# Kernel optimization log

Hardware: AMD Instinct MI355X
Metric: run time of the kernel (lower is better)

## Reference

```python
import jax, jax.numpy as jnp
import numpy as np

MARGIN = 0.2
NEG_INF = -1e30


def setup_inputs() -> dict:
    key = jax.random.key(0)
    k1, k2 = jax.random.split(key)
    B, D, C = 384, 256, 48
    features = jax.random.normal(k1, (B, D), dtype=jnp.float32)
    labels = jax.random.randint(k2, (B,), 0, C, dtype=jnp.int32)
    return {"features": features, "labels": labels, "epoch": 5}


def reference(features, labels, epoch):
    B = features.shape[0]
    # pairwise euclidean distance, clamped like torch.clamp(min=1e-11)
    diff = features[:, None, :] - features[None, :, :]          # [B,B,D]
    dist = jnp.sqrt(jnp.clip(jnp.sum(diff * diff, axis=-1), 1e-11))  # [B,B]

    idx = jnp.arange(B)
    same = labels[:, None] == labels[None, :]
    pos_mask = same & (idx[None, :] > idx[:, None])             # pairs (i,j), j>i, same label
    neg_mask = ~same

    # Gumbel-max sampling replaces the per-row np.random.choice host loop.
    gumbel = jax.random.gumbel(jax.random.key(42), (B, B, B), dtype=dist.dtype)

    if epoch > 3:
        # semi-hard negatives: pos_dist < d(i,k) < pos_dist + margin, weights 1/d(i,k)
        d_ik = dist[:, None, :]                                 # [B,1,B]
        d_pos = dist[:, :, None]                                # [B,B,1]
        semi = neg_mask[:, None, :] & (d_ik > d_pos) & (d_ik < d_pos + MARGIN)  # [B,B,B]
        logits = jnp.where(semi, -jnp.log(dist)[:, None, :], NEG_INF)  # log(1/d)
        has_neg = jnp.any(semi, axis=-1)                        # [B,B]
    else:
        # uniform random negative per (i,j) pair
        logits = jnp.where(neg_mask[:, None, :], 0.0, NEG_INF)  # [B,1,B]
        has_neg = jnp.broadcast_to(jnp.any(neg_mask, axis=-1)[:, None], (B, B))

    neg_idx = jnp.argmax(logits + gumbel, axis=-1)              # [B,B]
    neg_dist = jnp.take_along_axis(dist, neg_idx, axis=1)       # d(i, sampled_neg)

    valid = pos_mask & has_neg
    # MarginRankingLoss(neg, pos, target=1) = relu(pos - neg + margin)
    per_pair = jax.nn.relu(dist - neg_dist + MARGIN)
    count = jnp.sum(valid)
    total = jnp.sum(jnp.where(valid, per_pair, 0.0))
    return jnp.where(count > 0, total / jnp.maximum(count, 1), 0.0)
```

## Files before the change

kernel.cpp:

```cpp
#include <hip/hip_runtime.h>
#include <hip/hip_bf16.h>
#include <stdint.h>

#define BSZ 384
#define DD  256
#define NWAVES 6
#define NEG_BIG -3.0e38f

__device__ __forceinline__ void threefry_0_42(uint32_t c0, uint32_t c1,
                                              uint32_t& o0, uint32_t& o1) {
    const uint32_t k0 = 0u;
    const uint32_t k1 = 42u;
    const uint32_t k2 = 0u ^ 42u ^ 0x1BD11BDAu;
    uint32_t x0 = c0 + k0;
    uint32_t x1 = c1 + k1;
#define TF_RND(R) { x0 += x1; x1 = (x1 << (R)) | (x1 >> (32 - (R))); x1 ^= x0; }
    TF_RND(13) TF_RND(15) TF_RND(26) TF_RND(6)
    x0 += k1; x1 += k2 + 1u;
    TF_RND(17) TF_RND(29) TF_RND(16) TF_RND(24)
    x0 += k2; x1 += k0 + 2u;
    TF_RND(13) TF_RND(15) TF_RND(26) TF_RND(6)
    x0 += k0; x1 += k1 + 3u;
    TF_RND(17) TF_RND(29) TF_RND(16) TF_RND(24)
    x0 += k1; x1 += k2 + 4u;
    TF_RND(13) TF_RND(15) TF_RND(26) TF_RND(6)
    x0 += k2; x1 += k0 + 5u;
#undef TF_RND
    o0 = x0; o1 = x1;
}

__device__ __forceinline__ float gumbel_at(uint32_t idx) {
    uint32_t r0, r1;
    threefry_0_42(0u, idx, r0, r1);
    uint32_t bits = r0 ^ r1;
    uint32_t mant = bits >> 9;
    float f = __uint_as_float(mant | 0x3F800000u) - 1.0f;
    float u = (mant == 0u) ? 1.17549435e-38f : f;
    return -logf(-logf(u));
}

__global__ __launch_bounds__(BSZ) void fused_kernel(const float* __restrict__ F,
                                                    const int* __restrict__ labels,
                                                    const int* __restrict__ epochp,
                                                    float* __restrict__ total,
                                                    unsigned int* __restrict__ count,
                                                    unsigned int* __restrict__ done,
                                                    float* __restrict__ out) {
    __shared__ float    row[BSZ];
    __shared__ float    nlog[BSZ];
    __shared__ int      slab[BSZ];
    __shared__ int      plist[BSZ];
    __shared__ int      npos;
    __shared__ float    wtot[NWAVES];
    __shared__ unsigned wcnt[NWAVES];

    const int i    = blockIdx.x;
    const int tid  = threadIdx.x;
    const int wave = tid >> 6;
    const int lane = tid & 63;
    const int rl   = lane >> 3;
    const int s    = lane & 7;

    slab[tid] = labels[tid];
    if (tid == 0) npos = 0;
    __syncthreads();

    const int lab_i = slab[i];
    if (tid > i && slab[tid] == lab_i)
        plist[atomicAdd(&npos, 1)] = tid;
    const int  epoch   = *epochp;
    const bool semisel = (epoch > 3);
    __syncthreads();

    const int np = npos;
    float    t_total = 0.0f;
    unsigned t_count = 0u;

    if (np > 0) {
        const float4* F4 = (const float4*)F;

        float4 fi[8];
#pragma unroll
        for (int t = 0; t < 8; ++t) fi[t] = F4[i * (DD / 4) + t * 8 + s];

        for (int c = 0; c < 8; ++c) {
            const int k = c * 48 + wave * 8 + rl;
            const float4* fk = F4 + (size_t)k * (DD / 4);
            float a0 = 0.f, a1 = 0.f, a2 = 0.f, a3 = 0.f;
#pragma unroll
            for (int t = 0; t < 8; ++t) {
                float4 b = fk[t * 8 + s];
                float d0 = fi[t].x - b.x;
                float d1 = fi[t].y - b.y;
                float d2 = fi[t].z - b.z;
                float d3 = fi[t].w - b.w;
                a0 = fmaf(d0, d0, a0);
                a1 = fmaf(d1, d1, a1);
                a2 = fmaf(d2, d2, a2);
                a3 = fmaf(d3, d3, a3);
            }
            float p = (a0 + a1) + (a2 + a3);
            p += __shfl_down(p, 4, 64);
            p += __shfl_down(p, 2, 64);
            p += __shfl_down(p, 1, 64);
            if (s == 0) row[k] = sqrtf(fmaxf(p, 1e-11f));
        }
        __syncthreads();
        nlog[tid] = semisel ? -logf(row[tid]) : 0.0f;
        __syncthreads();

        for (int p = wave; p < np; p += NWAVES) {
            const int   j     = plist[p];
            const float d_pos = row[j];
            const float hi    = d_pos + 0.2f;
            float v  = NEG_BIG;
            int   kk = 0;
#pragma unroll
            for (int c = 0; c < BSZ / 64; ++c) {
                const int   k   = c * 64 + lane;
                const float dkk = row[k];
                const bool cand = (slab[k] != lab_i) &&
                                  (!semisel || (dkk > d_pos && dkk < hi));
                if (__any(cand)) {
                    if (cand) {
                        const uint32_t idx = (uint32_t)(i * BSZ + j) * (uint32_t)BSZ
                                             + (uint32_t)k;
                        float val = nlog[k] + gumbel_at(idx);
                        if (val > v) { v = val; kk = k; }
                    }
                }
            }
#pragma unroll
            for (int off = 32; off; off >>= 1) {
                float ov = __shfl_down(v, off, 64);
                int   oi = __shfl_down(kk, off, 64);
                if (ov > v || (ov == v && oi < kk)) { v = ov; kk = oi; }
            }
            if (lane == 0 && v > -1.0e38f) {
                t_total += fmaxf(d_pos - row[kk] + 0.2f, 0.0f);
                t_count += 1u;
            }
        }
    }

    if (lane == 0) { wtot[wave] = t_total; wcnt[wave] = t_count; }
    __syncthreads();
    if (tid == 0) {
        float    tt = 0.0f;
        unsigned cc = 0u;
#pragma unroll
        for (int q = 0; q < NWAVES; ++q) { tt += wtot[q]; cc += wcnt[q]; }
        if (cc) {
            atomicAdd(total, tt);
            atomicAdd(count, cc);
        }
        __threadfence();
        const unsigned prev = atomicAdd(done, 1u);
        if (prev == (unsigned)gridDim.x - 1u) {
            const float    T = atomicAdd(total, 0.0f);
            const unsigned C = atomicAdd(count, 0u);
            out[0] = (C > 0u) ? (T / (float)C) : 0.0f;
        }
    }
}

extern "C" void kernel_launch(void* const* d_in, const int* in_sizes, int n_in,
                              void* d_out, int out_size, void* d_ws, size_t ws_size,
                              hipStream_t stream) {
    const float* F      = (const float*)d_in[0];
    const int*   labels = (const int*)d_in[1];
    const int*   epoch  = (const int*)d_in[2];
    float*       out    = (float*)d_out;

    if (ws_size < 12) return;
    float*        total = (float*)d_ws;
    unsigned int* count = (unsigned int*)d_ws + 1;
    unsigned int* done  = (unsigned int*)d_ws + 2;

    hipMemsetAsync(d_ws, 0, 12, stream);
    fused_kernel<<<BSZ, BSZ, 0, stream>>>(F, labels, epoch, total, count, done, out);
}
```

Measured before the change: 79.01 us.

## Process two anchors per block and replace atomics with a reduction kernel

Each block now handles two anchor rows, so every loaded feature row k is reused for two distance computations. This halves the grid to 192 blocks and combines the positive-pair work of both anchors into one list. The global atomic accumulation, done-counter and memset are replaced by per-block slots plus a second single-wave reduction kernel. The costs are an extra kernel launch, higher register use, and fewer blocks to spread the Gumbel sampling work across the GPU.

```diff
diff --git a/kernel.cpp b/kernel.cpp
--- a/kernel.cpp
+++ b/kernel.cpp
@@ -5,6 +5,8 @@
 #define BSZ 384
 #define DD  256
 #define NWAVES 6
+#define NANCH 2
+#define NBLK (BSZ / NANCH)
 #define NEG_BIG -3.0e38f
 
 __device__ __forceinline__ void threefry_0_42(uint32_t c0, uint32_t c1,
@@ -42,19 +44,17 @@
 __global__ __launch_bounds__(BSZ) void fused_kernel(const float* __restrict__ F,
                                                     const int* __restrict__ labels,
                                                     const int* __restrict__ epochp,
-                                                    float* __restrict__ total,
-                                                    unsigned int* __restrict__ count,
-                                                    unsigned int* __restrict__ done,
-                                                    float* __restrict__ out) {
-    __shared__ float    row[BSZ];
-    __shared__ float    nlog[BSZ];
+                                                    float* __restrict__ tot_slot,
+                                                    unsigned int* __restrict__ cnt_slot) {
+    __shared__ float    row[NANCH][BSZ];
+    __shared__ float    nlog[NANCH][BSZ];
     __shared__ int      slab[BSZ];
-    __shared__ int      plist[BSZ];
+    __shared__ int      plist[NANCH * BSZ];
     __shared__ int      npos;
     __shared__ float    wtot[NWAVES];
     __shared__ unsigned wcnt[NWAVES];
 
-    const int i    = blockIdx.x;
+    const int i0   = blockIdx.x * NANCH;
     const int tid  = threadIdx.x;
     const int wave = tid >> 6;
     const int lane = tid & 63;
@@ -65,9 +65,10 @@
     if (tid == 0) npos = 0;
     __syncthreads();
 
-    const int lab_i = slab[i];
-    if (tid > i && slab[tid] == lab_i)
-        plist[atomicAdd(&npos, 1)] = tid;
+    const int lab0 = slab[i0];
+    const int lab1 = slab[i0 + 1];
+    if (tid > i0     && slab[tid] == lab0) plist[atomicAdd(&npos, 1)] = tid;
+    if (tid > i0 + 1 && slab[tid] == lab1) plist[atomicAdd(&npos, 1)] = (1 << 16) | tid;
     const int  epoch   = *epochp;
     const bool semisel = (epoch > 3);
     __syncthreads();
@@ -79,53 +80,65 @@
     if (np > 0) {
         const float4* F4 = (const float4*)F;
 
-        float4 fi[8];
-#pragma unroll
-        for (int t = 0; t < 8; ++t) fi[t] = F4[i * (DD / 4) + t * 8 + s];
+        float4 f0[8], f1[8];
+#pragma unroll
+        for (int t = 0; t < 8; ++t) {
+            f0[t] = F4[(i0    ) * (DD / 4) + t * 8 + s];
+            f1[t] = F4[(i0 + 1) * (DD / 4) + t * 8 + s];
+        }
 
         for (int c = 0; c < 8; ++c) {
             const int k = c * 48 + wave * 8 + rl;
             const float4* fk = F4 + (size_t)k * (DD / 4);
-            float a0 = 0.f, a1 = 0.f, a2 = 0.f, a3 = 0.f;
+            float a00 = 0.f, a01 = 0.f, a02 = 0.f, a03 = 0.f;
+            float a10 = 0.f, a11 = 0.f, a12 = 0.f, a13 = 0.f;
 #pragma unroll
             for (int t = 0; t < 8; ++t) {
                 float4 b = fk[t * 8 + s];
-                float d0 = fi[t].x - b.x;
-                float d1 = fi[t].y - b.y;
-                float d2 = fi[t].z - b.z;
-                float d3 = fi[t].w - b.w;
-                a0 = fmaf(d0, d0, a0);
-                a1 = fmaf(d1, d1, a1);
-                a2 = fmaf(d2, d2, a2);
-                a3 = fmaf(d3, d3, a3);
-            }
-            float p = (a0 + a1) + (a2 + a3);
-            p += __shfl_down(p, 4, 64);
-            p += __shfl_down(p, 2, 64);
-            p += __shfl_down(p, 1, 64);
-            if (s == 0) row[k] = sqrtf(fmaxf(p, 1e-11f));
+                float d0 = f0[t].x - b.x, d1 = f0[t].y - b.y;
+                float d2 = f0[t].z - b.z, d3 = f0[t].w - b.w;
+                a00 = fmaf(d0, d0, a00); a01 = fmaf(d1, d1, a01);
+                a02 = fmaf(d2, d2, a02); a03 = fmaf(d3, d3, a03);
+                float e0 = f1[t].x - b.x, e1 = f1[t].y - b.y;
+                float e2 = f1[t].z - b.z, e3 = f1[t].w - b.w;
+                a10 = fmaf(e0, e0, a10); a11 = fmaf(e1, e1, a11);
+                a12 = fmaf(e2, e2, a12); a13 = fmaf(e3, e3, a13);
+            }
+            float p0 = (a00 + a01) + (a02 + a03);
+            float p1 = (a10 + a11) + (a12 + a13);
+            p0 += __shfl_down(p0, 4, 64); p1 += __shfl_down(p1, 4, 64);
+            p0 += __shfl_down(p0, 2, 64); p1 += __shfl_down(p1, 2, 64);
+            p0 += __shfl_down(p0, 1, 64); p1 += __shfl_down(p1, 1, 64);
+            if (s == 0) {
+                row[0][k] = sqrtf(fmaxf(p0, 1e-11f));
+                row[1][k] = sqrtf(fmaxf(p1, 1e-11f));
+            }
         }
         __syncthreads();
-        nlog[tid] = semisel ? -logf(row[tid]) : 0.0f;
+        nlog[0][tid] = semisel ? -logf(row[0][tid]) : 0.0f;
+        nlog[1][tid] = semisel ? -logf(row[1][tid]) : 0.0f;
         __syncthreads();
 
         for (int p = wave; p < np; p += NWAVES) {
-            const int   j     = plist[p];
-            const float d_pos = row[j];
+            const int   pl    = plist[p];
+            const int   a     = pl >> 16;
+            const int   j     = pl & 0xFFFF;
+            const int   lab_a = a ? lab1 : lab0;
+            const float* rwa  = row[a];
+            const float d_pos = rwa[j];
             const float hi    = d_pos + 0.2f;
+            const uint32_t jb = (uint32_t)((i0 + a) * BSZ + j) * (uint32_t)BSZ;
             float v  = NEG_BIG;
             int   kk = 0;
 #pragma unroll
             for (int c = 0; c < BSZ / 64; ++c) {
                 const int   k   = c * 64 + lane;
-                const float dkk = row[k];
-                const bool cand = (slab[k] != lab_i) &&
+                const float dkk = rwa[k];
+                const bool cand = (slab[k] != lab_a) &&
                                   (!semisel || (dkk > d_pos && dkk < hi));
                 if (__any(cand)) {
                     if (cand) {
-                        const uint32_t idx = (uint32_t)(i * BSZ + j) * (uint32_t)BSZ
-                                             + (uint32_t)k;
-                        float val = nlog[k] + gumbel_at(idx);
+                        float val = nlog[a][k] + gumbel_at(jb + (uint32_t)k);
                         if (val > v) { v = val; kk = k; }
                     }
                 }
@@ -137,7 +150,7 @@
                 if (ov > v || (ov == v && oi < kk)) { v = ov; kk = oi; }
             }
             if (lane == 0 && v > -1.0e38f) {
-                t_total += fmaxf(d_pos - row[kk] + 0.2f, 0.0f);
+                t_total += fmaxf(d_pos - rwa[kk] + 0.2f, 0.0f);
                 t_count += 1u;
             }
         }
@@ -150,18 +163,28 @@
         unsigned cc = 0u;
 #pragma unroll
         for (int q = 0; q < NWAVES; ++q) { tt += wtot[q]; cc += wcnt[q]; }
-        if (cc) {
-            atomicAdd(total, tt);
-            atomicAdd(count, cc);
-        }
-        __threadfence();
-        const unsigned prev = atomicAdd(done, 1u);
-        if (prev == (unsigned)gridDim.x - 1u) {
-            const float    T = atomicAdd(total, 0.0f);
-            const unsigned C = atomicAdd(count, 0u);
-            out[0] = (C > 0u) ? (T / (float)C) : 0.0f;
-        }
-    }
+        tot_slot[blockIdx.x] = tt;
+        cnt_slot[blockIdx.x] = cc;
+    }
+}
+
+__global__ __launch_bounds__(64) void reduce_kernel(const float* __restrict__ tot_slot,
+                                                    const unsigned int* __restrict__ cnt_slot,
+                                                    float* __restrict__ out) {
+    const int lane = threadIdx.x;
+    float    t = 0.0f;
+    unsigned c = 0u;
+#pragma unroll
+    for (int q = 0; q < NBLK / 64; ++q) {
+        t += tot_slot[q * 64 + lane];
+        c += cnt_slot[q * 64 + lane];
+    }
+#pragma unroll
+    for (int off = 32; off; off >>= 1) {
+        t += __shfl_down(t, off, 64);
+        c += __shfl_down(c, off, 64);
+    }
+    if (lane == 0) out[0] = (c > 0u) ? (t / (float)c) : 0.0f;
 }
 
 extern "C" void kernel_launch(void* const* d_in, const int* in_sizes, int n_in,
@@ -172,11 +195,10 @@
     const int*   epoch  = (const int*)d_in[2];
     float*       out    = (float*)d_out;
 
-    if (ws_size < 12) return;
-    float*        total = (float*)d_ws;
-    unsigned int* count = (unsigned int*)d_ws + 1;
-    unsigned int* done  = (unsigned int*)d_ws + 2;
-
-    hipMemsetAsync(d_ws, 0, 12, stream);
-    fused_kernel<<<BSZ, BSZ, 0, stream>>>(F, labels, epoch, total, count, done, out);
-}
+    if (ws_size < 2 * NBLK * sizeof(float)) return;
+    float*        tot_slot = (float*)d_ws;
+    unsigned int* cnt_slot = (unsigned int*)d_ws + NBLK;
+
+    fused_kernel<<<NBLK, BSZ, 0, stream>>>(F, labels, epoch, tot_slot, cnt_slot);
+    reduce_kernel<<<1, 64, 0, stream>>>(tot_slot, cnt_slot, out);
+}
```

Measured after the change: 85.89 us. +8.7%, slower.
